# Kernel tuning notes

Hardware: AMD Instinct MI355X
Metric: run time of the kernel (lower is better)

The kernel has to match this reference:

```python
import jax, jax.numpy as jnp
import numpy as np

N_EMBD = 1024
N_HEAD = 16
HEAD_DIM = N_EMBD // N_HEAD
B, T = 2, 2048
EPS = 1e-5


def setup_inputs() -> dict:
    key = jax.random.key(0)
    ks = jax.random.split(key, 12)
    s = lambda fan_in: 1.0 / np.sqrt(fan_in)
    return {
        "x": jax.random.normal(ks[0], (B, T, N_EMBD), dtype=jnp.float32),
        "ln1_g": jnp.ones((N_EMBD,), jnp.float32),
        "ln1_b": jnp.zeros((N_EMBD,), jnp.float32),
        "W_attn": jax.random.normal(ks[1], (N_EMBD, 3 * N_EMBD), jnp.float32) * s(N_EMBD),
        "b_attn": jnp.zeros((3 * N_EMBD,), jnp.float32),
        "W_proj": jax.random.normal(ks[2], (N_EMBD, N_EMBD), jnp.float32) * s(N_EMBD),
        "b_proj": jnp.zeros((N_EMBD,), jnp.float32),
        "ln2_g": jnp.ones((N_EMBD,), jnp.float32),
        "ln2_b": jnp.zeros((N_EMBD,), jnp.float32),
        "W_fc": jax.random.normal(ks[3], (N_EMBD, 4 * N_EMBD), jnp.float32) * s(N_EMBD),
        "b_fc": jnp.zeros((4 * N_EMBD,), jnp.float32),
        "W_fc2": jax.random.normal(ks[4], (4 * N_EMBD, N_EMBD), jnp.float32) * s(4 * N_EMBD),
        "b_fc2": jnp.zeros((N_EMBD,), jnp.float32),
    }


def _layernorm(x, g, b):
    mu = jnp.mean(x, axis=-1, keepdims=True)
    var = jnp.mean(jnp.square(x - mu), axis=-1, keepdims=True)
    return (x - mu) * jax.lax.rsqrt(var + EPS) * g + b


def _attention(x, W_attn, b_attn, W_proj, b_proj):
    Bsz, Tlen, C = x.shape
    qkv = x @ W_attn + b_attn  # [B,T,3C]
    q, k, v = jnp.split(qkv, 3, axis=-1)
    # [B,H,T,D]
    q = q.reshape(Bsz, Tlen, N_HEAD, HEAD_DIM).transpose(0, 2, 1, 3)
    k = k.reshape(Bsz, Tlen, N_HEAD, HEAD_DIM).transpose(0, 2, 1, 3)
    v = v.reshape(Bsz, Tlen, N_HEAD, HEAD_DIM).transpose(0, 2, 1, 3)
    att = jnp.einsum("bhqd,bhkd->bhqk", q, k) * (HEAD_DIM ** -0.5)
    causal = jnp.tril(jnp.ones((Tlen, Tlen), dtype=bool))
    att = jnp.where(causal[None, None], att, -jnp.inf)
    att = jax.nn.softmax(att, axis=-1)
    y = jnp.einsum("bhqk,bhkd->bhqd", att, v)
    y = y.transpose(0, 2, 1, 3).reshape(Bsz, Tlen, C)
    return y @ W_proj + b_proj


def _mlp(x, W_fc, b_fc, W_fc2, b_fc2):
    h = jax.nn.gelu(x @ W_fc + b_fc, approximate=False)
    return h @ W_fc2 + b_fc2


def reference(x, ln1_g, ln1_b, W_attn, b_attn, W_proj, b_proj,
              ln2_g, ln2_b, W_fc, b_fc, W_fc2, b_fc2):
    x = x + _attention(_layernorm(x, ln1_g, ln1_b), W_attn, b_attn, W_proj, b_proj)
    x = x + _mlp(_layernorm(x, ln2_g, ln2_b), W_fc, b_fc, W_fc2, b_fc2)
    return x
```

## Files before the change

### kernel.cpp

```cpp
#include <hip/hip_runtime.h>
#include <math.h>

typedef unsigned short ushort_t;
typedef __attribute__((ext_vector_type(8))) short f16x8;
typedef __attribute__((ext_vector_type(4))) float f32x4;

#define N_EMBD 1024
#define N_HEAD 16
#define HEAD_DIM 64
#define SEQ_B 2
#define SEQ_T 2048
#define M_TOK (SEQ_B * SEQ_T)

__device__ __forceinline__ ushort_t f2b(float f) {
    union { float f; unsigned int u; } v; v.f = f;
    unsigned int r = (v.u + 0x7FFFu + ((v.u >> 16) & 1u)) >> 16;
    return (ushort_t)r;
}

__device__ __forceinline__ float gelu_fast(float v) {
    float u = v + 0.044715f * v * v * v;
    float e = __expf(-1.5957691216057308f * u);
    return v * __frcp_rn(1.0f + e);
}

__device__ __forceinline__ void gload_lds16(const ushort_t* g, ushort_t* l) {
    __builtin_amdgcn_global_load_lds(
        (const __attribute__((address_space(1))) void*)g,
        (__attribute__((address_space(3))) void*)l, 16, 0, 0);
}

__global__ __launch_bounds__(256) void prep_w(
    const float* __restrict__ Wa, const float* __restrict__ Wp,
    const float* __restrict__ Wf, const float* __restrict__ Wf2,
    ushort_t* __restrict__ Ta, ushort_t* __restrict__ Tp,
    ushort_t* __restrict__ Tf, ushort_t* __restrict__ Tf2,
    const float* __restrict__ x, const float* __restrict__ g1,
    const float* __restrict__ b1, ushort_t* __restrict__ xn) {
    int b = blockIdx.x;
    int t = threadIdx.x;
    if (b >= 12288) {
        int row = b - 12288;
        const float4 v = ((const float4*)(x + (size_t)row * N_EMBD))[t];
        float s = v.x + v.y + v.z + v.w;
        float s2 = v.x * v.x + v.y * v.y + v.z * v.z + v.w * v.w;
        for (int m = 1; m < 64; m <<= 1) {
            s += __shfl_xor(s, m, 64);
            s2 += __shfl_xor(s2, m, 64);
        }
        __shared__ float ss[4], ss2[4];
        if ((t & 63) == 0) { ss[t >> 6] = s; ss2[t >> 6] = s2; }
        __syncthreads();
        s = ss[0] + ss[1] + ss[2] + ss[3];
        s2 = ss2[0] + ss2[1] + ss2[2] + ss2[3];
        float mu = s * (1.0f / N_EMBD);
        float var = s2 * (1.0f / N_EMBD) - mu * mu;
        float rs = rsqrtf(var + 1e-5f);
        const float4 gg = ((const float4*)g1)[t];
        const float4 bb = ((const float4*)b1)[t];
        ushort_t o4[4];
        o4[0] = f2b((v.x - mu) * rs * gg.x + bb.x);
        o4[1] = f2b((v.y - mu) * rs * gg.y + bb.y);
        o4[2] = f2b((v.z - mu) * rs * gg.z + bb.z);
        o4[3] = f2b((v.w - mu) * rs * gg.w + bb.w);
        *(ushort4*)(xn + (size_t)row * N_EMBD + t * 4) = *(ushort4*)o4;
        return;
    }
    __shared__ float tile[32][33];
    const float* W; ushort_t* T; int K, N, nx;
    if (b < 3072)      { W = Wa;  T = Ta;  K = 1024; N = 3072; nx = 96; }
    else if (b < 4096) { W = Wp;  T = Tp;  K = 1024; N = 1024; nx = 32; b -= 3072; }
    else if (b < 8192) { W = Wf;  T = Tf;  K = 1024; N = 4096; nx = 128; b -= 4096; }
    else               { W = Wf2; T = Tf2; K = 4096; N = 1024; nx = 32; b -= 8192; }
    int n0 = (b % nx) * 32, k0 = (b / nx) * 32;
    for (int i = 0; i < 4; ++i) {
        int l = t + i * 256; int r = l >> 5, c2 = l & 31;
        tile[r][c2] = W[(size_t)(k0 + r) * N + n0 + c2];
    }
    __syncthreads();
    for (int i = 0; i < 4; ++i) {
        int l = t + i * 256; int r = l >> 5, c2 = l & 31;
        T[(size_t)(n0 + r) * K + k0 + c2] = f2b(tile[c2][r]);
    }
}

__global__ __launch_bounds__(256) void ln2_kernel(
    const float* __restrict__ x, const float* __restrict__ g,
    const float* __restrict__ b, ushort_t* __restrict__ out) {
    int row = blockIdx.x;
    int t = threadIdx.x;
    const float4 v = ((const float4*)(x + (size_t)row * N_EMBD))[t];
    float s = v.x + v.y + v.z + v.w;
    float s2 = v.x * v.x + v.y * v.y + v.z * v.z + v.w * v.w;
    for (int m = 1; m < 64; m <<= 1) {
        s += __shfl_xor(s, m, 64);
        s2 += __shfl_xor(s2, m, 64);
    }
    __shared__ float ss[4], ss2[4];
    if ((t & 63) == 0) { ss[t >> 6] = s; ss2[t >> 6] = s2; }
    __syncthreads();
    s = ss[0] + ss[1] + ss[2] + ss[3];
    s2 = ss2[0] + ss2[1] + ss2[2] + ss2[3];
    float mu = s * (1.0f / N_EMBD);
    float var = s2 * (1.0f / N_EMBD) - mu * mu;
    float rs = rsqrtf(var + 1e-5f);
    const float4 gg = ((const float4*)g)[t];
    const float4 bb = ((const float4*)b)[t];
    ushort_t o4[4];
    o4[0] = f2b((v.x - mu) * rs * gg.x + bb.x);
    o4[1] = f2b((v.y - mu) * rs * gg.y + bb.y);
    o4[2] = f2b((v.z - mu) * rs * gg.z + bb.z);
    o4[3] = f2b((v.w - mu) * rs * gg.w + bb.w);
    *(ushort4*)(out + (size_t)row * N_EMBD + t * 4) = *(ushort4*)o4;
}

template <int MODE, int NJ>
__device__ __forceinline__ void gemm_epilogue(
    f32x4 (&acc)[4][NJ], const float* __restrict__ bias,
    const float* __restrict__ resid, void* __restrict__ Cout,
    int m0, int n0, int wr, int wc, int quad, int l16, int N) {
    for (int i = 0; i < 4; ++i) {
        for (int j = 0; j < NJ; ++j) {
            int col = n0 + wc + j * 16 + l16;
            float bv = bias[col];
            for (int r = 0; r < 4; ++r) {
                int row = m0 + wr + i * 16 + quad * 4 + r;
                float v = acc[i][j][r] + bv;
                if (MODE == 2) v = gelu_fast(v);
                if (MODE == 1 || MODE == 3) v += resid[(size_t)row * N + col];
                if (MODE == 0 || MODE == 2)
                    ((ushort_t*)Cout)[(size_t)row * N + col] = f2b(v);
                else
                    ((float*)Cout)[(size_t)row * N + col] = v;
            }
        }
    }
}

template <int MODE>
__device__ __forceinline__ void gemm_body_dma(
    const ushort_t* __restrict__ A, const ushort_t* __restrict__ Bt,
    const float* __restrict__ bias, const float* __restrict__ resid,
    void* __restrict__ Cout, int M, int N, int K) {
    __shared__ ushort_t As[2][128 * 32];
    __shared__ ushort_t Bs[2][128 * 32];
    int t = threadIdx.x;
    int wave = t >> 6, lane = t & 63;
    int quad = lane >> 4, l16 = lane & 15;
    const int swl = (l16 ^ (l16 >> 2)) & 3;
    int wr = (wave >> 1) * 64, wc = (wave & 1) * 64;
    const int m0 = blockIdx.y * 128, n0 = blockIdx.x * 128;

    const int c = wave * 64 + lane;
    const int srow = c >> 2, s_l = c & 3;
    const int s_g = s_l ^ ((srow ^ (srow >> 2)) & 3);
    const ushort_t* Ap = &A[(size_t)(m0 + srow) * K + s_g * 8];
    const ushort_t* Bp = &Bt[(size_t)(n0 + srow) * K + s_g * 8];

    const int NK = K >> 5;
    gload_lds16(Ap, &As[0][wave * 512]);
    gload_lds16(Ap + (size_t)64 * K, &As[0][wave * 512 + 2048]);
    gload_lds16(Bp, &Bs[0][wave * 512]);
    gload_lds16(Bp + (size_t)64 * K, &Bs[0][wave * 512 + 2048]);

    f32x4 acc[4][4] = {};
    for (int kt = 0; kt < NK; ++kt) {
        const int cur = kt & 1;
        __syncthreads();
        if (kt + 1 < NK) {
            const int nxt = cur ^ 1;
            const int k0 = (kt + 1) << 5;
            gload_lds16(Ap + k0, &As[nxt][wave * 512]);
            gload_lds16(Ap + (size_t)64 * K + k0, &As[nxt][wave * 512 + 2048]);
            gload_lds16(Bp + k0, &Bs[nxt][wave * 512]);
            gload_lds16(Bp + (size_t)64 * K + k0, &Bs[nxt][wave * 512 + 2048]);
        }
        f16x8 af[4], bf[4];
        for (int i = 0; i < 4; ++i)
            af[i] = *(const f16x8*)&As[cur][(wr + i * 16 + l16) * 32 + (quad ^ swl) * 8];
        for (int j = 0; j < 4; ++j)
            bf[j] = *(const f16x8*)&Bs[cur][(wc + j * 16 + l16) * 32 + (quad ^ swl) * 8];
        for (int i = 0; i < 4; ++i)
            for (int j = 0; j < 4; ++j)
                acc[i][j] = __builtin_amdgcn_mfma_f32_16x16x32_bf16(
                    af[i], bf[j], acc[i][j], 0, 0, 0);
    }
    gemm_epilogue<MODE, 4>(acc, bias, resid, Cout, m0, n0, wr, wc, quad, l16, N);
}

template <int MODE>
__device__ __forceinline__ void gemm_body_splitk(
    const ushort_t* __restrict__ A, const ushort_t* __restrict__ Bt,
    const float* __restrict__ bias, const float* __restrict__ resid,
    void* __restrict__ Cout, int M, int N, int K) {
    __shared__ ushort_t As[2][2][128 * 32];
    __shared__ ushort_t Bs[2][2][64 * 32];
    int t = threadIdx.x;
    int wave = t >> 6, lane = t & 63;
    int half = wave >> 2, w4 = wave & 3;
    int quad = lane >> 4, l16 = lane & 15;
    const int swl = (l16 ^ (l16 >> 2)) & 3;
    int wr = (w4 >> 1) * 64, wc = (w4 & 1) * 32;
    const int m0 = blockIdx.y * 128, n0 = blockIdx.x * 64;

    const int K2 = K >> 1;
    const int c = w4 * 64 + lane;
    const int srow = c >> 2, s_l = c & 3;
    const int s_g = s_l ^ ((srow ^ (srow >> 2)) & 3);
    const ushort_t* Ap = &A[(size_t)(m0 + srow) * K + (size_t)half * K2 + s_g * 8];
    const ushort_t* Bp = &Bt[(size_t)(n0 + srow) * K + (size_t)half * K2 + s_g * 8];

    const int NK = K2 >> 5;
    gload_lds16(Ap, &As[0][half][w4 * 512]);
    gload_lds16(Ap + (size_t)64 * K, &As[0][half][w4 * 512 + 2048]);
    gload_lds16(Bp, &Bs[0][half][w4 * 512]);

    f32x4 acc[4][2] = {};
    for (int kt = 0; kt < NK; ++kt) {
        const int cur = kt & 1;
        __syncthreads();
        if (kt + 1 < NK) {
            const int nxt = cur ^ 1;
            const int k0 = (kt + 1) << 5;
            gload_lds16(Ap + k0, &As[nxt][half][w4 * 512]);
            gload_lds16(Ap + (size_t)64 * K + k0, &As[nxt][half][w4 * 512 + 2048]);
            gload_lds16(Bp + k0, &Bs[nxt][half][w4 * 512]);
        }
        f16x8 af[4], bf[2];
        for (int i = 0; i < 4; ++i)
            af[i] = *(const f16x8*)&As[cur][half][(wr + i * 16 + l16) * 32 + (quad ^ swl) * 8];
        for (int j = 0; j < 2; ++j)
            bf[j] = *(const f16x8*)&Bs[cur][half][(wc + j * 16 + l16) * 32 + (quad ^ swl) * 8];
        for (int i = 0; i < 4; ++i)
            for (int j = 0; j < 2; ++j)
                acc[i][j] = __builtin_amdgcn_mfma_f32_16x16x32_bf16(
                    af[i], bf[j], acc[i][j], 0, 0, 0);
    }
    __syncthreads();
    float* red = (float*)&As[0][0][0];
    if (half == 1) {
        for (int i = 0; i < 4; ++i)
            for (int j = 0; j < 2; ++j)
                for (int r = 0; r < 4; ++r)
                    red[(wr + i * 16 + quad * 4 + r) * 64 + wc + j * 16 + l16] =
                        acc[i][j][r];
    }
    __syncthreads();
    if (half == 0) {
        for (int i = 0; i < 4; ++i)
            for (int j = 0; j < 2; ++j)
                for (int r = 0; r < 4; ++r)
                    acc[i][j][r] +=
                        red[(wr + i * 16 + quad * 4 + r) * 64 + wc + j * 16 + l16];
        gemm_epilogue<MODE, 2>(acc, bias, resid, Cout, m0, n0, wr, wc, quad, l16, N);
    }
}

__global__ __launch_bounds__(256) void gemm_qkv(
    const ushort_t* A, const ushort_t* Bt, const float* bias, void* C,
    int M, int N, int K) { gemm_body_dma<0>(A, Bt, bias, nullptr, C, M, N, K); }
__global__ __launch_bounds__(256) void gemm_mlp1(
    const ushort_t* A, const ushort_t* Bt, const float* bias, void* C,
    int M, int N, int K) { gemm_body_dma<2>(A, Bt, bias, nullptr, C, M, N, K); }
__global__ __launch_bounds__(512) void gemm_proj(
    const ushort_t* A, const ushort_t* Bt, const float* bias,
    const float* resid, void* C, int M, int N, int K) {
    gemm_body_splitk<1>(A, Bt, bias, resid, C, M, N, K); }
__global__ __launch_bounds__(512) void gemm_out(
    const ushort_t* A, const ushort_t* Bt, const float* bias,
    const float* resid, void* C, int M, int N, int K) {
    gemm_body_splitk<3>(A, Bt, bias, resid, C, M, N, K); }

__global__ __launch_bounds__(256) void attn_kernel(
    const ushort_t* __restrict__ qkv, ushort_t* __restrict__ y) {
    const int bh = blockIdx.y;
    const int b = bh >> 4, h = bh & 15;
    const int tok0 = b * SEQ_T;
    const int t = threadIdx.x, wave = t >> 6, lane = t & 63;
    const int quad = lane >> 4, l16 = lane & 15;
    const int sw8 = l16 & 7;
    const size_t ld = 3 * N_EMBD;
    const ushort_t* Qb = qkv + (size_t)tok0 * ld + h * HEAD_DIM;
    const ushort_t* Kb = Qb + N_EMBD;
    const ushort_t* Vb = Qb + 2 * N_EMBD;

    __shared__ ushort_t Ks[64 * 64];
    __shared__ ushort_t Vt[64 * 64];
    __shared__ ushort_t Pl[4][16 * 64];

    const int kc = wave * 64 + lane;
    const int kv_s = kc >> 3, ks_l = kc & 7;
    const int ks_g = ks_l ^ (kv_s & 7);
    const ushort_t* KpL = Kb + (size_t)kv_s * ld + ks_g * 8;

    f16x8 onesB;
    for (int i = 0; i < 8; ++i) onesB[i] = (short)0x3F80;

    for (int phase = 0; phase < 2; ++phase) {
        const int qt = phase == 0 ? (int)blockIdx.x : 31 - (int)blockIdx.x;
        const int q0 = qt * 64;

        const int qrow = q0 + wave * 16 + l16;
        f16x8 qf0 = *(const f16x8*)&Qb[(size_t)qrow * ld + quad * 8];
        f16x8 qf1 = *(const f16x8*)&Qb[(size_t)qrow * ld + 32 + quad * 8];

        f32x4 o[4] = {};
        f32x4 lsum = {};

        const int nkt = qt + 1;
        for (int kt = 0; kt < nkt; ++kt) {
            __syncthreads();
            const ushort_t* kp = KpL + (size_t)kt * 64 * ld;
            gload_lds16(kp, &Ks[wave * 512]);
            gload_lds16(kp + (size_t)32 * ld, &Ks[wave * 512 + 2048]);
            for (int i = 0; i < 2; ++i) {
                int l = t + i * 256;
                int kv = l >> 3, dc = (l & 7) * 8;
                uint4 raw = *(const uint4*)&Vb[(size_t)(kt * 64 + kv) * ld + dc];
                const ushort_t* pv = (const ushort_t*)&raw;
                int pos = kv ^ ((l & 7) << 3);
                for (int e = 0; e < 8; ++e)
                    Vt[(dc + e) * 64 + pos] = pv[e];
            }
            __syncthreads();
            f32x4 s[4];
            const int ksl = (quad ^ sw8) * 8;
            for (int j = 0; j < 4; ++j) {
                const int kr = j * 16 + l16;
                f16x8 kf0 = *(const f16x8*)&Ks[kr * 64 + ksl];
                f16x8 kf1 = *(const f16x8*)&Ks[kr * 64 + (ksl ^ 32)];
                f32x4 z = {};
                z = __builtin_amdgcn_mfma_f32_16x16x32_bf16(qf0, kf0, z, 0, 0, 0);
                z = __builtin_amdgcn_mfma_f32_16x16x32_bf16(qf1, kf1, z, 0, 0, 0);
                s[j] = z;
            }
            if (kt == qt) {
                const int qr = wave * 16 + quad * 4;
                for (int j = 0; j < 4; ++j) {
                    int kg = j * 16 + l16;
                    for (int r = 0; r < 4; ++r)
                        if (kg > qr + r) s[j][r] = -INFINITY;
                }
            }
            ushort_t* myP = Pl[wave];
            for (int j = 0; j < 4; ++j) {
                int kvv = j * 16 + l16;
                int slotb = ((kvv >> 3) * 8);
                int klo = kvv & 7;
                for (int r = 0; r < 4; ++r) {
                    float p = __expf(__builtin_fmaf(s[j][r], 0.125f, -20.0f));
                    int q = quad * 4 + r;
                    myP[q * 64 + (slotb ^ ((q & 7) * 8)) + klo] = f2b(p);
                }
            }
            const int psl = (quad ^ sw8) * 8;
            f16x8 pa0 = *(const f16x8*)&myP[l16 * 64 + psl];
            f16x8 pa1 = *(const f16x8*)&myP[l16 * 64 + (psl ^ 32)];
            lsum = __builtin_amdgcn_mfma_f32_16x16x32_bf16(pa0, onesB, lsum, 0, 0, 0);
            lsum = __builtin_amdgcn_mfma_f32_16x16x32_bf16(pa1, onesB, lsum, 0, 0, 0);
            for (int dj = 0; dj < 4; ++dj) {
                const int d = dj * 16 + l16;
                const int dsw = ((d >> 3) & 7) * 8;
                f16x8 vb0 = *(const f16x8*)&Vt[d * 64 + ((quad * 8) ^ dsw)];
                f16x8 vb1 = *(const f16x8*)&Vt[d * 64 + (((quad * 8) ^ dsw) ^ 32)];
                f32x4 oo = o[dj];
                oo = __builtin_amdgcn_mfma_f32_16x16x32_bf16(pa0, vb0, oo, 0, 0, 0);
                oo = __builtin_amdgcn_mfma_f32_16x16x32_bf16(pa1, vb1, oo, 0, 0, 0);
                o[dj] = oo;
            }
        }
        float rl[4];
        for (int r = 0; r < 4; ++r) rl[r] = __frcp_rn(lsum[r]);
        for (int dj = 0; dj < 4; ++dj)
            for (int r = 0; r < 4; ++r) {
                int row = tok0 + q0 + wave * 16 + quad * 4 + r;
                int col = h * HEAD_DIM + dj * 16 + l16;
                y[(size_t)row * N_EMBD + col] = f2b(o[dj][r] * rl[r]);
            }
    }
}

extern "C" void kernel_launch(void* const* d_in, const int* in_sizes, int n_in,
                              void* d_out, int out_size, void* d_ws, size_t ws_size,
                              hipStream_t stream) {
    const float* x      = (const float*)d_in[0];
    const float* ln1_g  = (const float*)d_in[1];
    const float* ln1_b  = (const float*)d_in[2];
    const float* W_attn = (const float*)d_in[3];
    const float* b_attn = (const float*)d_in[4];
    const float* W_proj = (const float*)d_in[5];
    const float* b_proj = (const float*)d_in[6];
    const float* ln2_g  = (const float*)d_in[7];
    const float* ln2_b  = (const float*)d_in[8];
    const float* W_fc   = (const float*)d_in[9];
    const float* b_fc   = (const float*)d_in[10];
    const float* W_fc2  = (const float*)d_in[11];
    const float* b_fc2  = (const float*)d_in[12];
    float* out = (float*)d_out;

    char* w = (char*)d_ws;
    size_t o = 0;
    ushort_t* xn      = (ushort_t*)(w + o); o += (size_t)M_TOK * N_EMBD * 2;
    ushort_t* qkv     = (ushort_t*)(w + o); o += (size_t)M_TOK * 3 * N_EMBD * 2;
    ushort_t* y       = (ushort_t*)(w + o); o += (size_t)M_TOK * N_EMBD * 2;
    float*    x1      = (float*)(w + o);    o += (size_t)M_TOK * N_EMBD * 4;
    ushort_t* x1n     = (ushort_t*)(w + o); o += (size_t)M_TOK * N_EMBD * 2;
    ushort_t* hbuf    = (ushort_t*)(w + o); o += (size_t)M_TOK * 4 * N_EMBD * 2;
    ushort_t* Wt_attn = (ushort_t*)(w + o); o += (size_t)N_EMBD * 3 * N_EMBD * 2;
    ushort_t* Wt_proj = (ushort_t*)(w + o); o += (size_t)N_EMBD * N_EMBD * 2;
    ushort_t* Wt_fc   = (ushort_t*)(w + o); o += (size_t)N_EMBD * 4 * N_EMBD * 2;
    ushort_t* Wt_fc2  = (ushort_t*)(w + o); o += (size_t)4 * N_EMBD * N_EMBD * 2;

    prep_w<<<12288 + M_TOK, 256, 0, stream>>>(
        W_attn, W_proj, W_fc, W_fc2, Wt_attn, Wt_proj, Wt_fc, Wt_fc2,
        x, ln1_g, ln1_b, xn);
    gemm_qkv<<<dim3(3 * N_EMBD / 128, M_TOK / 128), 256, 0, stream>>>(
        xn, Wt_attn, b_attn, qkv, M_TOK, 3 * N_EMBD, N_EMBD);
    attn_kernel<<<dim3(SEQ_T / 128, SEQ_B * N_HEAD), 256, 0, stream>>>(qkv, y);
    gemm_proj<<<dim3(N_EMBD / 64, M_TOK / 128), 512, 0, stream>>>(
        y, Wt_proj, b_proj, x, x1, M_TOK, N_EMBD, N_EMBD);
    ln2_kernel<<<M_TOK, 256, 0, stream>>>(x1, ln2_g, ln2_b, x1n);
    gemm_mlp1<<<dim3(4 * N_EMBD / 128, M_TOK / 128), 256, 0, stream>>>(
        x1n, Wt_fc, b_fc, hbuf, M_TOK, 4 * N_EMBD, N_EMBD);
    gemm_out<<<dim3(N_EMBD / 64, M_TOK / 128), 512, 0, stream>>>(
        hbuf, Wt_fc2, b_fc2, x1, out, M_TOK, N_EMBD, 4 * N_EMBD);
    (void)in_sizes; (void)n_in; (void)out_size; (void)ws_size;
}
```

Baseline: 362.5 us.

## Triple-buffer GEMM LDS pipeline and double-buffer K/V in attention

The GEMM bodies move from two LDS stages to three, prefetching two k-tiles ahead. The per-iteration __syncthreads is replaced by an inline-asm partial vmcnt wait plus barrier, so the tile after next can stay in flight while the current one is consumed. The attention kernel double-buffers K and V tiles, issuing the next tile's loads before computing on the current one, and raises MFMA priority with s_setprio. It also drops the paired-phase causal load balancing in favour of one q-tile per block on a doubled grid. The costs are more LDS per block, which can lower occupancy, reliance on exact vmcnt counts for correctness, and causal imbalance across attention blocks.

```diff
diff --git a/kernel.cpp b/kernel.cpp
--- a/kernel.cpp
+++ b/kernel.cpp
@@ -29,6 +29,10 @@
         (const __attribute__((address_space(1))) void*)g,
         (__attribute__((address_space(3))) void*)l, 16, 0, 0);
 }
+
+#define PIPE_BAR_4() asm volatile("s_waitcnt vmcnt(4) lgkmcnt(0)\n\ts_barrier" ::: "memory")
+#define PIPE_BAR_3() asm volatile("s_waitcnt vmcnt(3) lgkmcnt(0)\n\ts_barrier" ::: "memory")
+#define PIPE_BAR_0() asm volatile("s_waitcnt vmcnt(0) lgkmcnt(0)\n\ts_barrier" ::: "memory")
 
 __global__ __launch_bounds__(256) void prep_w(
     const float* __restrict__ Wa, const float* __restrict__ Wp,
@@ -142,8 +146,8 @@
     const ushort_t* __restrict__ A, const ushort_t* __restrict__ Bt,
     const float* __restrict__ bias, const float* __restrict__ resid,
     void* __restrict__ Cout, int M, int N, int K) {
-    __shared__ ushort_t As[2][128 * 32];
-    __shared__ ushort_t Bs[2][128 * 32];
+    __shared__ ushort_t As[3][128 * 32];
+    __shared__ ushort_t Bs[3][128 * 32];
     int t = threadIdx.x;
     int wave = t >> 6, lane = t & 63;
     int quad = lane >> 4, l16 = lane & 15;
@@ -158,22 +162,24 @@
     const ushort_t* Bp = &Bt[(size_t)(n0 + srow) * K + s_g * 8];
 
     const int NK = K >> 5;
-    gload_lds16(Ap, &As[0][wave * 512]);
-    gload_lds16(Ap + (size_t)64 * K, &As[0][wave * 512 + 2048]);
-    gload_lds16(Bp, &Bs[0][wave * 512]);
-    gload_lds16(Bp + (size_t)64 * K, &Bs[0][wave * 512 + 2048]);
+    for (int p = 0; p < 2; ++p) {
+        const int k0 = p << 5;
+        gload_lds16(Ap + k0, &As[p][wave * 512]);
+        gload_lds16(Ap + (size_t)64 * K + k0, &As[p][wave * 512 + 2048]);
+        gload_lds16(Bp + k0, &Bs[p][wave * 512]);
+        gload_lds16(Bp + (size_t)64 * K + k0, &Bs[p][wave * 512 + 2048]);
+    }
 
     f32x4 acc[4][4] = {};
+    int cur = 0, pre = 2;
     for (int kt = 0; kt < NK; ++kt) {
-        const int cur = kt & 1;
-        __syncthreads();
-        if (kt + 1 < NK) {
-            const int nxt = cur ^ 1;
-            const int k0 = (kt + 1) << 5;
-            gload_lds16(Ap + k0, &As[nxt][wave * 512]);
-            gload_lds16(Ap + (size_t)64 * K + k0, &As[nxt][wave * 512 + 2048]);
-            gload_lds16(Bp + k0, &Bs[nxt][wave * 512]);
-            gload_lds16(Bp + (size_t)64 * K + k0, &Bs[nxt][wave * 512 + 2048]);
+        if (kt + 1 < NK) PIPE_BAR_4(); else PIPE_BAR_0();
+        if (kt + 2 < NK) {
+            const int k0 = (kt + 2) << 5;
+            gload_lds16(Ap + k0, &As[pre][wave * 512]);
+            gload_lds16(Ap + (size_t)64 * K + k0, &As[pre][wave * 512 + 2048]);
+            gload_lds16(Bp + k0, &Bs[pre][wave * 512]);
+            gload_lds16(Bp + (size_t)64 * K + k0, &Bs[pre][wave * 512 + 2048]);
         }
         f16x8 af[4], bf[4];
         for (int i = 0; i < 4; ++i)
@@ -184,6 +190,8 @@
             for (int j = 0; j < 4; ++j)
                 acc[i][j] = __builtin_amdgcn_mfma_f32_16x16x32_bf16(
                     af[i], bf[j], acc[i][j], 0, 0, 0);
+        cur = (cur == 2) ? 0 : cur + 1;
+        pre = (pre == 2) ? 0 : pre + 1;
     }
     gemm_epilogue<MODE, 4>(acc, bias, resid, Cout, m0, n0, wr, wc, quad, l16, N);
 }
@@ -193,8 +201,8 @@
     const ushort_t* __restrict__ A, const ushort_t* __restrict__ Bt,
     const float* __restrict__ bias, const float* __restrict__ resid,
     void* __restrict__ Cout, int M, int N, int K) {
-    __shared__ ushort_t As[2][2][128 * 32];
-    __shared__ ushort_t Bs[2][2][64 * 32];
+    __shared__ ushort_t As[3][2][128 * 32];
+    __shared__ ushort_t Bs[3][2][64 * 32];
     int t = threadIdx.x;
     int wave = t >> 6, lane = t & 63;
     int half = wave >> 2, w4 = wave & 3;
@@ -211,20 +219,22 @@
     const ushort_t* Bp = &Bt[(size_t)(n0 + srow) * K + (size_t)half * K2 + s_g * 8];
 
     const int NK = K2 >> 5;
-    gload_lds16(Ap, &As[0][half][w4 * 512]);
-    gload_lds16(Ap + (size_t)64 * K, &As[0][half][w4 * 512 + 2048]);
-    gload_lds16(Bp, &Bs[0][half][w4 * 512]);
+    for (int p = 0; p < 2; ++p) {
+        const int k0 = p << 5;
+        gload_lds16(Ap + k0, &As[p][half][w4 * 512]);
+        gload_lds16(Ap + (size_t)64 * K + k0, &As[p][half][w4 * 512 + 2048]);
+        gload_lds16(Bp + k0, &Bs[p][half][w4 * 512]);
+    }
 
     f32x4 acc[4][2] = {};
+    int cur = 0, pre = 2;
     for (int kt = 0; kt < NK; ++kt) {
-        const int cur = kt & 1;
-        __syncthreads();
-        if (kt + 1 < NK) {
-            const int nxt = cur ^ 1;
-            const int k0 = (kt + 1) << 5;
-            gload_lds16(Ap + k0, &As[nxt][half][w4 * 512]);
-            gload_lds16(Ap + (size_t)64 * K + k0, &As[nxt][half][w4 * 512 + 2048]);
-            gload_lds16(Bp + k0, &Bs[nxt][half][w4 * 512]);
+        if (kt + 1 < NK) PIPE_BAR_3(); else PIPE_BAR_0();
+        if (kt + 2 < NK) {
+            const int k0 = (kt + 2) << 5;
+            gload_lds16(Ap + k0, &As[pre][half][w4 * 512]);
+            gload_lds16(Ap + (size_t)64 * K + k0, &As[pre][half][w4 * 512 + 2048]);
+            gload_lds16(Bp + k0, &Bs[pre][half][w4 * 512]);
         }
         f16x8 af[4], bf[2];
         for (int i = 0; i < 4; ++i)
@@ -235,6 +245,8 @@
             for (int j = 0; j < 2; ++j)
                 acc[i][j] = __builtin_amdgcn_mfma_f32_16x16x32_bf16(
                     af[i], bf[j], acc[i][j], 0, 0, 0);
+        cur = (cur == 2) ? 0 : cur + 1;
+        pre = (pre == 2) ? 0 : pre + 1;
     }
     __syncthreads();
     float* red = (float*)&As[0][0][0];
@@ -284,8 +296,8 @@
     const ushort_t* Kb = Qb + N_EMBD;
     const ushort_t* Vb = Qb + 2 * N_EMBD;
 
-    __shared__ ushort_t Ks[64 * 64];
-    __shared__ ushort_t Vt[64 * 64];
+    __shared__ ushort_t Ks[2][64 * 64];
+    __shared__ ushort_t Vt[2][64 * 64];
     __shared__ ushort_t Pl[4][16 * 64];
 
     const int kc = wave * 64 + lane;
@@ -293,91 +305,114 @@
     const int ks_g = ks_l ^ (kv_s & 7);
     const ushort_t* KpL = Kb + (size_t)kv_s * ld + ks_g * 8;
 
+    const int v_kv0 = t >> 3, v_dc0 = (t & 7) * 8;
+    const int v_pos0 = v_kv0 ^ ((t & 7) << 3);
+    const int v_kv1 = (t + 256) >> 3, v_dc1 = v_dc0;
+    const int v_pos1 = v_kv1 ^ ((t & 7) << 3);
+
     f16x8 onesB;
     for (int i = 0; i < 8; ++i) onesB[i] = (short)0x3F80;
 
-    for (int phase = 0; phase < 2; ++phase) {
-        const int qt = phase == 0 ? (int)blockIdx.x : 31 - (int)blockIdx.x;
-        const int q0 = qt * 64;
-
-        const int qrow = q0 + wave * 16 + l16;
-        f16x8 qf0 = *(const f16x8*)&Qb[(size_t)qrow * ld + quad * 8];
-        f16x8 qf1 = *(const f16x8*)&Qb[(size_t)qrow * ld + 32 + quad * 8];
-
-        f32x4 o[4] = {};
-        f32x4 lsum = {};
-
-        const int nkt = qt + 1;
-        for (int kt = 0; kt < nkt; ++kt) {
-            __syncthreads();
-            const ushort_t* kp = KpL + (size_t)kt * 64 * ld;
-            gload_lds16(kp, &Ks[wave * 512]);
-            gload_lds16(kp + (size_t)32 * ld, &Ks[wave * 512 + 2048]);
-            for (int i = 0; i < 2; ++i) {
-                int l = t + i * 256;
-                int kv = l >> 3, dc = (l & 7) * 8;
-                uint4 raw = *(const uint4*)&Vb[(size_t)(kt * 64 + kv) * ld + dc];
-                const ushort_t* pv = (const ushort_t*)&raw;
-                int pos = kv ^ ((l & 7) << 3);
-                for (int e = 0; e < 8; ++e)
-                    Vt[(dc + e) * 64 + pos] = pv[e];
+    const int qt = blockIdx.x;
+    const int q0 = qt * 64;
+
+    const int qrow = q0 + wave * 16 + l16;
+    f16x8 qf0 = *(const f16x8*)&Qb[(size_t)qrow * ld + quad * 8];
+    f16x8 qf1 = *(const f16x8*)&Qb[(size_t)qrow * ld + 32 + quad * 8];
+
+    f32x4 o[4] = {};
+    f32x4 lsum = {};
+
+    const int nkt = qt + 1;
+
+    gload_lds16(KpL, &Ks[0][wave * 512]);
+    gload_lds16(KpL + (size_t)32 * ld, &Ks[0][wave * 512 + 2048]);
+    {
+        uint4 r0 = *(const uint4*)&Vb[(size_t)v_kv0 * ld + v_dc0];
+        uint4 r1 = *(const uint4*)&Vb[(size_t)v_kv1 * ld + v_dc1];
+        const ushort_t* p0 = (const ushort_t*)&r0;
+        const ushort_t* p1 = (const ushort_t*)&r1;
+        for (int e = 0; e < 8; ++e) Vt[0][(v_dc0 + e) * 64 + v_pos0] = p0[e];
+        for (int e = 0; e < 8; ++e) Vt[0][(v_dc1 + e) * 64 + v_pos1] = p1[e];
+    }
+
+    for (int kt = 0; kt < nkt; ++kt) {
+        const int cur = kt & 1;
+        __syncthreads();
+        const bool pf = (kt + 1 < nkt);
+        uint4 vr0, vr1;
+        if (pf) {
+            vr0 = *(const uint4*)&Vb[(size_t)((kt + 1) * 64 + v_kv0) * ld + v_dc0];
+            vr1 = *(const uint4*)&Vb[(size_t)((kt + 1) * 64 + v_kv1) * ld + v_dc1];
+            const ushort_t* kp = KpL + (size_t)(kt + 1) * 64 * ld;
+            gload_lds16(kp, &Ks[cur ^ 1][wave * 512]);
+            gload_lds16(kp + (size_t)32 * ld, &Ks[cur ^ 1][wave * 512 + 2048]);
+        }
+        f32x4 s[4];
+        const int ksl = (quad ^ sw8) * 8;
+        __builtin_amdgcn_s_setprio(1);
+        for (int j = 0; j < 4; ++j) {
+            const int kr = j * 16 + l16;
+            f16x8 kf0 = *(const f16x8*)&Ks[cur][kr * 64 + ksl];
+            f16x8 kf1 = *(const f16x8*)&Ks[cur][kr * 64 + (ksl ^ 32)];
+            f32x4 z = {};
+            z = __builtin_amdgcn_mfma_f32_16x16x32_bf16(qf0, kf0, z, 0, 0, 0);
+            z = __builtin_amdgcn_mfma_f32_16x16x32_bf16(qf1, kf1, z, 0, 0, 0);
+            s[j] = z;
+        }
+        __builtin_amdgcn_s_setprio(0);
+        if (kt == qt) {
+            const int qr = wave * 16 + quad * 4;
+            for (int j = 0; j < 4; ++j) {
+                int kg = j * 16 + l16;
+                for (int r = 0; r < 4; ++r)
+                    if (kg > qr + r) s[j][r] = -INFINITY;
             }
-            __syncthreads();
-            f32x4 s[4];
-            const int ksl = (quad ^ sw8) * 8;
-            for (int j = 0; j < 4; ++j) {
-                const int kr = j * 16 + l16;
-                f16x8 kf0 = *(const f16x8*)&Ks[kr * 64 + ksl];
-                f16x8 kf1 = *(const f16x8*)&Ks[kr * 64 + (ksl ^ 32)];
-                f32x4 z = {};
-                z = __builtin_amdgcn_mfma_f32_16x16x32_bf16(qf0, kf0, z, 0, 0, 0);
-                z = __builtin_amdgcn_mfma_f32_16x16x32_bf16(qf1, kf1, z, 0, 0, 0);
-                s[j] = z;
+        }
+        ushort_t* myP = Pl[wave];
+        for (int j = 0; j < 4; ++j) {
+            int kvv = j * 16 + l16;
+            int slotb = ((kvv >> 3) * 8);
+            int klo = kvv & 7;
+            for (int r = 0; r < 4; ++r) {
+                float p = __expf(__builtin_fmaf(s[j][r], 0.125f, -20.0f));
+                int q = quad * 4 + r;
+                myP[q * 64 + (slotb ^ ((q & 7) * 8)) + klo] = f2b(p);
             }
-            if (kt == qt) {
-                const int qr = wave * 16 + quad * 4;
-                for (int j = 0; j < 4; ++j) {
-                    int kg = j * 16 + l16;
-                    for (int r = 0; r < 4; ++r)
-                        if (kg > qr + r) s[j][r] = -INFINITY;
-                }
-            }
-            ushort_t* myP = Pl[wave];
-            for (int j = 0; j < 4; ++j) {
-                int kvv = j * 16 + l16;
-                int slotb = ((kvv >> 3) * 8);
-                int klo = kvv & 7;
-                for (int r = 0; r < 4; ++r) {
-                    float p = __expf(__builtin_fmaf(s[j][r], 0.125f, -20.0f));
-                    int q = quad * 4 + r;
-                    myP[q * 64 + (slotb ^ ((q & 7) * 8)) + klo] = f2b(p);
-                }
-            }
-            const int psl = (quad ^ sw8) * 8;
-            f16x8 pa0 = *(const f16x8*)&myP[l16 * 64 + psl];
-            f16x8 pa1 = *(const f16x8*)&myP[l16 * 64 + (psl ^ 32)];
-            lsum = __builtin_amdgcn_mfma_f32_16x16x32_bf16(pa0, onesB, lsum, 0, 0, 0);
-            lsum = __builtin_amdgcn_mfma_f32_16x16x32_bf16(pa1, onesB, lsum, 0, 0, 0);
-            for (int dj = 0; dj < 4; ++dj) {
-                const int d = dj * 16 + l16;
-                const int dsw = ((d >> 3) & 7) * 8;
-                f16x8 vb0 = *(const f16x8*)&Vt[d * 64 + ((quad * 8) ^ dsw)];
-                f16x8 vb1 = *(const f16x8*)&Vt[d * 64 + (((quad * 8) ^ dsw) ^ 32)];
-                f32x4 oo = o[dj];
-                oo = __builtin_amdgcn_mfma_f32_16x16x32_bf16(pa0, vb0, oo, 0, 0, 0);
-                oo = __builtin_amdgcn_mfma_f32_16x16x32_bf16(pa1, vb1, oo, 0, 0, 0);
-                o[dj] = oo;
-            }
-        }
-        float rl[4];
-        for (int r = 0; r < 4; ++r) rl[r] = __frcp_rn(lsum[r]);
-        for (int dj = 0; dj < 4; ++dj)
-            for (int r = 0; r < 4; ++r) {
-                int row = tok0 + q0 + wave * 16 + quad * 4 + r;
-                int col = h * HEAD_DIM + dj * 16 + l16;
-                y[(size_t)row * N_EMBD + col] = f2b(o[dj][r] * rl[r]);
-            }
-    }
+        }
+        const int psl = (quad ^ sw8) * 8;
+        f16x8 pa0 = *(const f16x8*)&myP[l16 * 64 + psl];
+        f16x8 pa1 = *(const f16x8*)&myP[l16 * 64 + (psl ^ 32)];
+        __builtin_amdgcn_s_setprio(1);
+        lsum = __builtin_amdgcn_mfma_f32_16x16x32_bf16(pa0, onesB, lsum, 0, 0, 0);
+        lsum = __builtin_amdgcn_mfma_f32_16x16x32_bf16(pa1, onesB, lsum, 0, 0, 0);
+        for (int dj = 0; dj < 4; ++dj) {
+            const int d = dj * 16 + l16;
+            const int dsw = ((d >> 3) & 7) * 8;
+            f16x8 vb0 = *(const f16x8*)&Vt[cur][d * 64 + ((quad * 8) ^ dsw)];
+            f16x8 vb1 = *(const f16x8*)&Vt[cur][d * 64 + (((quad * 8) ^ dsw) ^ 32)];
+            f32x4 oo = o[dj];
+            oo = __builtin_amdgcn_mfma_f32_16x16x32_bf16(pa0, vb0, oo, 0, 0, 0);
+            oo = __builtin_amdgcn_mfma_f32_16x16x32_bf16(pa1, vb1, oo, 0, 0, 0);
+            o[dj] = oo;
+        }
+        __builtin_amdgcn_s_setprio(0);
+        if (pf) {
+            const ushort_t* p0 = (const ushort_t*)&vr0;
+            const ushort_t* p1 = (const ushort_t*)&vr1;
+            ushort_t* Vn = Vt[cur ^ 1];
+            for (int e = 0; e < 8; ++e) Vn[(v_dc0 + e) * 64 + v_pos0] = p0[e];
+            for (int e = 0; e < 8; ++e) Vn[(v_dc1 + e) * 64 + v_pos1] = p1[e];
+        }
+    }
+    float rl[4];
+    for (int r = 0; r < 4; ++r) rl[r] = __frcp_rn(lsum[r]);
+    for (int dj = 0; dj < 4; ++dj)
+        for (int r = 0; r < 4; ++r) {
+            int row = tok0 + q0 + wave * 16 + quad * 4 + r;
+            int col = h * HEAD_DIM + dj * 16 + l16;
+            y[(size_t)row * N_EMBD + col] = f2b(o[dj][r] * rl[r]);
+        }
 }
 
 extern "C" void kernel_launch(void* const* d_in, const int* in_sizes, int n_in,
@@ -416,7 +451,7 @@
         x, ln1_g, ln1_b, xn);
     gemm_qkv<<<dim3(3 * N_EMBD / 128, M_TOK / 128), 256, 0, stream>>>(
         xn, Wt_attn, b_attn, qkv, M_TOK, 3 * N_EMBD, N_EMBD);
-    attn_kernel<<<dim3(SEQ_T / 128, SEQ_B * N_HEAD), 256, 0, stream>>>(qkv, y);
+    attn_kernel<<<dim3(SEQ_T / 64, SEQ_B * N_HEAD), 256, 0, stream>>>(qkv, y);
     gemm_proj<<<dim3(N_EMBD / 64, M_TOK / 128), 512, 0, stream>>>(
         y, Wt_proj, b_proj, x, x1, M_TOK, N_EMBD, N_EMBD);
     ln2_kernel<<<M_TOK, 256, 0, stream>>>(x1, ln2_g, ln2_b, x1n);
```

Measured after the change: 409.3 us. 1.13x slower.

## Double-buffer 128-key tiles in attention with prefetched K/V and wave priority

Applied to the files above, without the earlier changes.

Widens each attention key/value tile from 64 to 128 keys and double-buffers K in LDS. The next tile's K is loaded asynchronously and its V is held in registers, then written to the transposed V buffer after a barrier. This overlaps global loads with the MFMA work and halves the number of loop iterations and block barriers. It also raises wave priority around the MFMA sections. In exchange it uses more LDS, which may lower occupancy. On diagonal tiles it wastes some compute on up to 64 fully masked keys.

```diff
diff --git a/kernel.cpp b/kernel.cpp
--- a/kernel.cpp
+++ b/kernel.cpp
@@ -284,21 +284,30 @@
     const ushort_t* Kb = Qb + N_EMBD;
     const ushort_t* Vb = Qb + 2 * N_EMBD;
 
-    __shared__ ushort_t Ks[64 * 64];
-    __shared__ ushort_t Vt[64 * 64];
-    __shared__ ushort_t Pl[4][16 * 64];
+    __shared__ ushort_t Ks[2][128 * 64];
+    __shared__ ushort_t Vt[64 * 136];
+    __shared__ ushort_t Pl[4][16 * 128];
 
     const int kc = wave * 64 + lane;
     const int kv_s = kc >> 3, ks_l = kc & 7;
     const int ks_g = ks_l ^ (kv_s & 7);
     const ushort_t* KpL = Kb + (size_t)kv_s * ld + ks_g * 8;
 
+    const int v_dcI = t & 7, v_dc = v_dcI * 8;
+    int v_kv[4], v_pos[4];
+    for (int i = 0; i < 4; ++i) {
+        int l = t + i * 256;
+        v_kv[i] = l >> 3;
+        v_pos[i] = v_kv[i] ^ (v_dcI << 3);
+    }
+
     f16x8 onesB;
     for (int i = 0; i < 8; ++i) onesB[i] = (short)0x3F80;
 
     for (int phase = 0; phase < 2; ++phase) {
         const int qt = phase == 0 ? (int)blockIdx.x : 31 - (int)blockIdx.x;
         const int q0 = qt * 64;
+        const int nkt = (q0 + 191) >> 7;
 
         const int qrow = q0 + wave * 16 + l16;
         f16x8 qf0 = *(const f16x8*)&Qb[(size_t)qrow * ld + quad * 8];
@@ -307,66 +316,87 @@
         f32x4 o[4] = {};
         f32x4 lsum = {};
 
-        const int nkt = qt + 1;
+        __syncthreads();
+        gload_lds16(KpL, &Ks[0][wave * 512]);
+        gload_lds16(KpL + (size_t)32 * ld, &Ks[0][wave * 512 + 2048]);
+        gload_lds16(KpL + (size_t)64 * ld, &Ks[0][wave * 512 + 4096]);
+        gload_lds16(KpL + (size_t)96 * ld, &Ks[0][wave * 512 + 6144]);
+        for (int i = 0; i < 4; ++i) {
+            uint4 r = *(const uint4*)&Vb[(size_t)v_kv[i] * ld + v_dc];
+            const ushort_t* pv = (const ushort_t*)&r;
+            for (int e = 0; e < 8; ++e)
+                Vt[(v_dc + e) * 136 + v_pos[i]] = pv[e];
+        }
+
         for (int kt = 0; kt < nkt; ++kt) {
+            const int cur = kt & 1;
             __syncthreads();
-            const ushort_t* kp = KpL + (size_t)kt * 64 * ld;
-            gload_lds16(kp, &Ks[wave * 512]);
-            gload_lds16(kp + (size_t)32 * ld, &Ks[wave * 512 + 2048]);
-            for (int i = 0; i < 2; ++i) {
-                int l = t + i * 256;
-                int kv = l >> 3, dc = (l & 7) * 8;
-                uint4 raw = *(const uint4*)&Vb[(size_t)(kt * 64 + kv) * ld + dc];
-                const ushort_t* pv = (const ushort_t*)&raw;
-                int pos = kv ^ ((l & 7) << 3);
-                for (int e = 0; e < 8; ++e)
-                    Vt[(dc + e) * 64 + pos] = pv[e];
-            }
-            __syncthreads();
-            f32x4 s[4];
-            const int ksl = (quad ^ sw8) * 8;
-            for (int j = 0; j < 4; ++j) {
+            const bool pf = (kt + 1 < nkt);
+            uint4 vr[4];
+            if (pf) {
+                for (int i = 0; i < 4; ++i)
+                    vr[i] = *(const uint4*)&Vb[(size_t)((kt + 1) * 128 + v_kv[i]) * ld + v_dc];
+                const ushort_t* kp = KpL + (size_t)(kt + 1) * 128 * ld;
+                gload_lds16(kp, &Ks[cur ^ 1][wave * 512]);
+                gload_lds16(kp + (size_t)32 * ld, &Ks[cur ^ 1][wave * 512 + 2048]);
+                gload_lds16(kp + (size_t)64 * ld, &Ks[cur ^ 1][wave * 512 + 4096]);
+                gload_lds16(kp + (size_t)96 * ld, &Ks[cur ^ 1][wave * 512 + 6144]);
+            }
+            f32x4 s[8];
+            const int ksl = (quad ^ sw8) << 3;
+            __builtin_amdgcn_s_setprio(1);
+            for (int j = 0; j < 8; ++j) {
                 const int kr = j * 16 + l16;
-                f16x8 kf0 = *(const f16x8*)&Ks[kr * 64 + ksl];
-                f16x8 kf1 = *(const f16x8*)&Ks[kr * 64 + (ksl ^ 32)];
+                f16x8 kf0 = *(const f16x8*)&Ks[cur][kr * 64 + ksl];
+                f16x8 kf1 = *(const f16x8*)&Ks[cur][kr * 64 + (ksl ^ 32)];
                 f32x4 z = {};
                 z = __builtin_amdgcn_mfma_f32_16x16x32_bf16(qf0, kf0, z, 0, 0, 0);
                 z = __builtin_amdgcn_mfma_f32_16x16x32_bf16(qf1, kf1, z, 0, 0, 0);
                 s[j] = z;
             }
-            if (kt == qt) {
-                const int qr = wave * 16 + quad * 4;
-                for (int j = 0; j < 4; ++j) {
-                    int kg = j * 16 + l16;
+            __builtin_amdgcn_s_setprio(0);
+            if (kt == nkt - 1) {
+                const int qg = q0 + wave * 16 + quad * 4;
+                for (int j = 0; j < 8; ++j) {
+                    int kg = kt * 128 + j * 16 + l16;
                     for (int r = 0; r < 4; ++r)
-                        if (kg > qr + r) s[j][r] = -INFINITY;
+                        if (kg > qg + r) s[j][r] = -INFINITY;
                 }
             }
             ushort_t* myP = Pl[wave];
-            for (int j = 0; j < 4; ++j) {
+            for (int j = 0; j < 8; ++j) {
                 int kvv = j * 16 + l16;
-                int slotb = ((kvv >> 3) * 8);
-                int klo = kvv & 7;
+                int chunk = kvv >> 3, klo = kvv & 7;
                 for (int r = 0; r < 4; ++r) {
                     float p = __expf(__builtin_fmaf(s[j][r], 0.125f, -20.0f));
                     int q = quad * 4 + r;
-                    myP[q * 64 + (slotb ^ ((q & 7) * 8)) + klo] = f2b(p);
+                    myP[q * 128 + ((chunk ^ (q & 7)) << 3) + klo] = f2b(p);
                 }
             }
-            const int psl = (quad ^ sw8) * 8;
-            f16x8 pa0 = *(const f16x8*)&myP[l16 * 64 + psl];
-            f16x8 pa1 = *(const f16x8*)&myP[l16 * 64 + (psl ^ 32)];
-            lsum = __builtin_amdgcn_mfma_f32_16x16x32_bf16(pa0, onesB, lsum, 0, 0, 0);
-            lsum = __builtin_amdgcn_mfma_f32_16x16x32_bf16(pa1, onesB, lsum, 0, 0, 0);
+            f16x8 pa[4];
+            for (int ks = 0; ks < 4; ++ks)
+                pa[ks] = *(const f16x8*)&myP[l16 * 128 + ((((ks << 2) | quad) ^ sw8) << 3)];
+            __builtin_amdgcn_s_setprio(1);
+            for (int ks = 0; ks < 4; ++ks)
+                lsum = __builtin_amdgcn_mfma_f32_16x16x32_bf16(pa[ks], onesB, lsum, 0, 0, 0);
             for (int dj = 0; dj < 4; ++dj) {
                 const int d = dj * 16 + l16;
-                const int dsw = ((d >> 3) & 7) * 8;
-                f16x8 vb0 = *(const f16x8*)&Vt[d * 64 + ((quad * 8) ^ dsw)];
-                f16x8 vb1 = *(const f16x8*)&Vt[d * 64 + (((quad * 8) ^ dsw) ^ 32)];
+                const int dsw3 = (d >> 3) & 7;
                 f32x4 oo = o[dj];
-                oo = __builtin_amdgcn_mfma_f32_16x16x32_bf16(pa0, vb0, oo, 0, 0, 0);
-                oo = __builtin_amdgcn_mfma_f32_16x16x32_bf16(pa1, vb1, oo, 0, 0, 0);
+                for (int ks = 0; ks < 4; ++ks) {
+                    f16x8 vb = *(const f16x8*)&Vt[d * 136 + ((((ks << 2) | quad) ^ dsw3) << 3)];
+                    oo = __builtin_amdgcn_mfma_f32_16x16x32_bf16(pa[ks], vb, oo, 0, 0, 0);
+                }
                 o[dj] = oo;
+            }
+            __builtin_amdgcn_s_setprio(0);
+            if (pf) {
+                asm volatile("s_barrier" ::: "memory");
+                for (int i = 0; i < 4; ++i) {
+                    const ushort_t* pv = (const ushort_t*)&vr[i];
+                    for (int e = 0; e < 8; ++e)
+                        Vt[(v_dc + e) * 136 + v_pos[i]] = pv[e];
+                }
             }
         }
         float rl[4];
```

Measured after the change: 361.8 us. Within noise of the previous version (-0.2%).
